# Performance work log

Hardware: AMD Instinct MI355X
Metric: run time of the kernel (lower is better)

The kernel has to match this reference:

```python
import jax, jax.numpy as jnp
import numpy as np

N = 65536      # batch rows
D = 32         # input_dim (number of per-feature sub-MLPs)
H = 128        # nodes_per_layer_in_sub_fn
# num_hidden_layers_per_feature_fn = 2 -> Linear(1,H),ReLU, Linear(H,H),ReLU, Linear(H,1)


def setup_inputs() -> dict:
    key = jax.random.key(0)
    ks = jax.random.split(key, 7)
    s1 = 1.0            # fan_in=1 kaiming-uniform-ish scale
    sH = 1.0 / np.sqrt(H)
    x = jax.random.normal(ks[0], (N, D), dtype=jnp.float32)
    W1 = jax.random.uniform(ks[1], (D, H), jnp.float32, -s1, s1)      # Linear(1,H) weight per feature
    b1 = jax.random.uniform(ks[2], (D, H), jnp.float32, -s1, s1)
    W2 = jax.random.uniform(ks[3], (D, H, H), jnp.float32, -sH, sH)   # Linear(H,H) per feature
    b2 = jax.random.uniform(ks[4], (D, H), jnp.float32, -sH, sH)
    W3 = jax.random.uniform(ks[5], (D, H), jnp.float32, -sH, sH)      # Linear(H,1) per feature
    b3 = jax.random.uniform(ks[6], (D,), jnp.float32, -sH, sH)
    return {"x": x, "W1": W1, "b1": b1, "W2": W2, "b2": b2, "W3": W3, "b3": b3}


def reference(x, W1, b1, W2, b2, W3, b3):
    # h1[n,d,h] = relu(x[n,d] * W1[d,h] + b1[d,h])
    h1 = jax.nn.relu(x[:, :, None] * W1[None, :, :] + b1[None, :, :])          # [N,D,H]
    # h2: per-feature batched GEMM, Linear(H,H) + ReLU
    h2 = jax.nn.relu(jnp.einsum('ndh,dhk->ndk', h1, W2) + b2[None, :, :])      # [N,D,H]
    # per-feature output Linear(H,1), then sum across features, keepdim
    per_feat = jnp.einsum('ndh,dh->nd', h2, W3) + b3[None, :]                  # [N,D]
    return jnp.sum(per_feat, axis=1, keepdims=True)                            # [N,1]
```

## Files before the change

### kernel.cpp

```cpp
#include <hip/hip_runtime.h>
#include <hip/hip_bf16.h>
#include <stdint.h>


#define D_FEAT 32
#define H_DIM  128
#define SLOTS  16
#define THREADS 256
#define RPB    4096
#define ITERS  32

typedef float    f32x16 __attribute__((ext_vector_type(16)));
typedef short    bf16x8 __attribute__((ext_vector_type(8)));
typedef uint32_t u32;

static __device__ __forceinline__ u32 cvtpk(float lo, float hi) {
    u32 r;
    asm("v_cvt_pk_bf16_f32 %0, %1, %2" : "=v"(r) : "v"(lo), "v"(hi));
    return r;
}
static __device__ __forceinline__ bf16x8 frag4(u32 a, u32 b, u32 c, u32 d) {
    int4 t = make_int4((int)a, (int)b, (int)c, (int)d);
    return __builtin_bit_cast(bf16x8, t);
}
static __device__ __forceinline__ bf16x8 frag1(u32 a) { return frag4(a, 0u, 0u, 0u); }

#define MFMA32(A, B, C) __builtin_amdgcn_mfma_f32_32x32x16_bf16((A), (B), (C), 0, 0, 0)

static __device__ __forceinline__ bf16x8 relu_pack(const f32x16& v, int s) {
    u32 c0 = cvtpk(fmaxf(v[8*s+0], 0.f), fmaxf(v[8*s+1], 0.f));
    u32 c1 = cvtpk(fmaxf(v[8*s+2], 0.f), fmaxf(v[8*s+3], 0.f));
    u32 c2 = cvtpk(fmaxf(v[8*s+4], 0.f), fmaxf(v[8*s+5], 0.f));
    u32 c3 = cvtpk(fmaxf(v[8*s+6], 0.f), fmaxf(v[8*s+7], 0.f));
    return frag4(c0, c1, c2, c3);
}

__global__ __launch_bounds__(256) void kan_init_out(const float* __restrict__ b3,
                                                    float* __restrict__ out, int n) {
    int i = blockIdx.x * blockDim.x + threadIdx.x;
    float s = 0.f;
#pragma unroll
    for (int k = 0; k < D_FEAT; ++k) s += b3[k];
    if (i < n) out[i] = s;
}

__global__ __launch_bounds__(THREADS, 2) void kan_main(
    const float* __restrict__ x,
    const float* __restrict__ W1,
    const float* __restrict__ b1,
    const float* __restrict__ W2,
    const float* __restrict__ b2,
    const float* __restrict__ W3,
    float* __restrict__ out)
{
    __shared__ float xall[RPB];
    __shared__ u32 w3lds[2][8][4];

    const int tid   = threadIdx.x;
    const int d     = blockIdx.x / SLOTS;
    const int bslot = blockIdx.x % SLOTS;
    const int w     = tid >> 6;
    const int l     = tid & 63;
    const int l31   = l & 31;
    const int g     = l >> 5;
    const size_t rowbase = (size_t)bslot * RPB;

#pragma unroll
    for (int i = 0; i < RPB / THREADS; ++i) {
        int idx = tid + THREADS * i;
        xall[idx] = x[(rowbase + idx) * D_FEAT + d];
    }
    if (tid < 16) {
        int gg = tid >> 3, ks2 = tid & 7;
        const float* W3d = W3 + d * H_DIM;
#pragma unroll
        for (int p = 0; p < 4; ++p) {
            int e0 = 2 * p, e1 = 2 * p + 1;
            int k0 = 16 * ks2 + 4 * gg + (e0 & 3) + 8 * (e0 >> 2);
            int k1 = 16 * ks2 + 4 * gg + (e1 & 3) + 8 * (e1 >> 2);
            w3lds[gg][ks2][p] = cvtpk(W3d[k0], W3d[k1]);
        }
    }

    u32 w1b1[4], b2w[4];
#pragma unroll
    for (int mt = 0; mt < 4; ++mt) {
        int m = 32 * mt + l31;
        u32 v  = cvtpk(W1[d * H_DIM + m], b1[d * H_DIM + m]);
        u32 bb = cvtpk(b2[d * H_DIM + m], 0.0f);
        w1b1[mt] = g ? 0u : v;
        b2w[mt]  = g ? 0u : bb;
    }
    const u32 onesw = g ? 0u : 0x00003F80u;

    bf16x8 w2f[4][8];
    {
        const float* W2d = W2 + (size_t)d * H_DIM * H_DIM;
#pragma unroll
        for (int mo = 0; mo < 4; ++mo) {
            int mm = 32 * mo + l31;
#pragma unroll
            for (int ks = 0; ks < 8; ++ks) {
                u32 dw[4];
#pragma unroll
                for (int p = 0; p < 4; ++p) {
                    int e0 = 2 * p, e1 = 2 * p + 1;
                    int k0 = 16 * ks + 4 * g + (e0 & 3) + 8 * (e0 >> 2);
                    int k1 = 16 * ks + 4 * g + (e1 & 3) + 8 * (e1 >> 2);
                    dw[p] = cvtpk(W2d[(size_t)k0 * H_DIM + mm],
                                  W2d[(size_t)k1 * H_DIM + mm]);
                }
                w2f[mo][ks] = frag4(dw[0], dw[1], dw[2], dw[3]);
            }
        }
    }
    __syncthreads();

    const f32x16 zc = {};

    for (int t = 0; t < ITERS; ++t) {
        const int loff = t * 128 + 32 * w;
        float xv = xall[loff + l31];
        u32 xpk = g ? 0u : cvtpk(xv, 1.0f);
        bf16x8 Bx = frag1(xpk);

        bf16x8 bfr[8];
#pragma unroll
        for (int mt = 0; mt < 4; ++mt) {
            f32x16 d1 = MFMA32(frag1(w1b1[mt]), Bx, zc);
            bfr[2 * mt + 0] = relu_pack(d1, 0);
            bfr[2 * mt + 1] = relu_pack(d1, 1);
        }

        f32x16 acc2 = zc;
        const bf16x8 onesB = frag1(onesw);
#pragma unroll
        for (int pa = 0; pa < 2; ++pa) {
            f32x16 a0 = MFMA32(frag1(b2w[2 * pa + 0]), onesB, zc);
            f32x16 a1 = MFMA32(frag1(b2w[2 * pa + 1]), onesB, zc);
#pragma unroll
            for (int ks = 0; ks < 8; ++ks) {
                a0 = MFMA32(w2f[2 * pa + 0][ks], bfr[ks], a0);
                a1 = MFMA32(w2f[2 * pa + 1][ks], bfr[ks], a1);
            }
            {
                const int mo0 = 2 * pa + 0, mo1 = 2 * pa + 1;
                bf16x8 w3a, w3b, w3c, w3d;
                w3a = *reinterpret_cast<const bf16x8*>(&w3lds[g][2 * mo0 + 0][0]);
                w3b = *reinterpret_cast<const bf16x8*>(&w3lds[g][2 * mo0 + 1][0]);
                w3c = *reinterpret_cast<const bf16x8*>(&w3lds[g][2 * mo1 + 0][0]);
                w3d = *reinterpret_cast<const bf16x8*>(&w3lds[g][2 * mo1 + 1][0]);
                acc2 = MFMA32(w3a, relu_pack(a0, 0), acc2);
                acc2 = MFMA32(w3b, relu_pack(a0, 1), acc2);
                acc2 = MFMA32(w3c, relu_pack(a1, 0), acc2);
                acc2 = MFMA32(w3d, relu_pack(a1, 1), acc2);
            }
        }
        if (!g) atomicAdd(&out[rowbase + loff + l31], acc2[0]);
    }
}

extern "C" void kernel_launch(void* const* d_in, const int* in_sizes, int n_in,
                              void* d_out, int out_size, void* d_ws, size_t ws_size,
                              hipStream_t stream) {
    const float* x  = (const float*)d_in[0];
    const float* W1 = (const float*)d_in[1];
    const float* b1 = (const float*)d_in[2];
    const float* W2 = (const float*)d_in[3];
    const float* b2 = (const float*)d_in[4];
    const float* W3 = (const float*)d_in[5];
    const float* b3 = (const float*)d_in[6];
    float* out = (float*)d_out;
    const int N = in_sizes[0] / D_FEAT;

    kan_init_out<<<(N + 255) / 256, 256, 0, stream>>>(b3, out, N);
    kan_main<<<D_FEAT * SLOTS, THREADS, 0, stream>>>(x, W1, b1, W2, b2, W3, out);
}
```

Baseline: 157.1 us.

## Split output channels across waves, interleave layer GEMMs, replace W3 MFMA with FMA reduction

Each wave now holds only half of W2's output tiles (2 of 4 mo blocks), and two waves share a 32-row tile. This halves register pressure and raises occupancy to 3 blocks and 24 slots per feature. The layer-1 MFMA is interleaved with the layer-2 MFMAs, and the final W3 projection uses scalar FMAs plus a cross-half shuffle instead of extra MFMAs. The b3 init kernel is replaced by a memset, with b3 folded into the atomics from one block group. In exchange, the atomicAdd count doubles, each wave recomputes layer 1, and the row-tile distribution across blocks is uneven.

```diff
diff --git a/kernel.cpp b/kernel.cpp
--- a/kernel.cpp
+++ b/kernel.cpp
@@ -5,10 +5,10 @@
 
 #define D_FEAT 32
 #define H_DIM  128
-#define SLOTS  16
+#define SLOTS  24
 #define THREADS 256
-#define RPB    4096
-#define ITERS  32
+#define ROWTILES 1024
+#define MAXT   43
 
 typedef float    f32x16 __attribute__((ext_vector_type(16)));
 typedef short    bf16x8 __attribute__((ext_vector_type(8)));
@@ -35,70 +35,59 @@
     return frag4(c0, c1, c2, c3);
 }
 
-__global__ __launch_bounds__(256) void kan_init_out(const float* __restrict__ b3,
-                                                    float* __restrict__ out, int n) {
-    int i = blockIdx.x * blockDim.x + threadIdx.x;
-    float s = 0.f;
-#pragma unroll
-    for (int k = 0; k < D_FEAT; ++k) s += b3[k];
-    if (i < n) out[i] = s;
-}
-
-__global__ __launch_bounds__(THREADS, 2) void kan_main(
+__global__ __launch_bounds__(THREADS, 3) void kan_main(
     const float* __restrict__ x,
     const float* __restrict__ W1,
     const float* __restrict__ b1,
     const float* __restrict__ W2,
     const float* __restrict__ b2,
     const float* __restrict__ W3,
+    const float* __restrict__ b3,
     float* __restrict__ out)
 {
-    __shared__ float xall[RPB];
-    __shared__ u32 w3lds[2][8][4];
+    __shared__ float xall[MAXT * 64];
+    __shared__ float W3s[H_DIM];
 
     const int tid   = threadIdx.x;
     const int d     = blockIdx.x / SLOTS;
     const int bslot = blockIdx.x % SLOTS;
     const int w     = tid >> 6;
+    const int wm    = w >> 1;
+    const int wn    = w & 1;
     const int l     = tid & 63;
     const int l31   = l & 31;
     const int g     = l >> 5;
-    const size_t rowbase = (size_t)bslot * RPB;
 
+    const int ntile = (ROWTILES - 1 - bslot) / SLOTS + 1;
+
+    for (int idx = tid; idx < ntile * 64; idx += THREADS) {
+        int tl = idx >> 6;
+        xall[idx] = x[(size_t)((bslot + SLOTS * tl) * 64 + (idx & 63)) * D_FEAT + d];
+    }
+    if (tid < H_DIM) W3s[tid] = W3[d * H_DIM + tid];
+
+    float b3s = 0.f;
 #pragma unroll
-    for (int i = 0; i < RPB / THREADS; ++i) {
-        int idx = tid + THREADS * i;
-        xall[idx] = x[(rowbase + idx) * D_FEAT + d];
-    }
-    if (tid < 16) {
-        int gg = tid >> 3, ks2 = tid & 7;
-        const float* W3d = W3 + d * H_DIM;
-#pragma unroll
-        for (int p = 0; p < 4; ++p) {
-            int e0 = 2 * p, e1 = 2 * p + 1;
-            int k0 = 16 * ks2 + 4 * gg + (e0 & 3) + 8 * (e0 >> 2);
-            int k1 = 16 * ks2 + 4 * gg + (e1 & 3) + 8 * (e1 >> 2);
-            w3lds[gg][ks2][p] = cvtpk(W3d[k0], W3d[k1]);
-        }
-    }
+    for (int k = 0; k < D_FEAT; ++k) b3s += b3[k];
 
-    u32 w1b1[4], b2w[4];
+    const int mo0 = 2 * wm, mo1 = 2 * wm + 1;
+    u32 w1b1[4], b2w[2];
 #pragma unroll
     for (int mt = 0; mt < 4; ++mt) {
         int m = 32 * mt + l31;
-        u32 v  = cvtpk(W1[d * H_DIM + m], b1[d * H_DIM + m]);
-        u32 bb = cvtpk(b2[d * H_DIM + m], 0.0f);
+        u32 v = cvtpk(W1[d * H_DIM + m], b1[d * H_DIM + m]);
         w1b1[mt] = g ? 0u : v;
-        b2w[mt]  = g ? 0u : bb;
     }
-    const u32 onesw = g ? 0u : 0x00003F80u;
+    b2w[0] = g ? 0u : cvtpk(b2[d * H_DIM + 32 * mo0 + l31], 0.f);
+    b2w[1] = g ? 0u : cvtpk(b2[d * H_DIM + 32 * mo1 + l31], 0.f);
+    const bf16x8 onesB = frag1(g ? 0u : 0x00003F80u);
 
-    bf16x8 w2f[4][8];
+    bf16x8 w2f[2][8];
     {
         const float* W2d = W2 + (size_t)d * H_DIM * H_DIM;
 #pragma unroll
-        for (int mo = 0; mo < 4; ++mo) {
-            int mm = 32 * mo + l31;
+        for (int j = 0; j < 2; ++j) {
+            int mm = 32 * (mo0 + j) + l31;
 #pragma unroll
             for (int ks = 0; ks < 8; ++ks) {
                 u32 dw[4];
@@ -110,53 +99,51 @@
                     dw[p] = cvtpk(W2d[(size_t)k0 * H_DIM + mm],
                                   W2d[(size_t)k1 * H_DIM + mm]);
                 }
-                w2f[mo][ks] = frag4(dw[0], dw[1], dw[2], dw[3]);
+                w2f[j][ks] = frag4(dw[0], dw[1], dw[2], dw[3]);
             }
         }
     }
     __syncthreads();
 
     const f32x16 zc = {};
+    const bool addb3 = (d == 0) && (wm == 0);
 
-    for (int t = 0; t < ITERS; ++t) {
-        const int loff = t * 128 + 32 * w;
-        float xv = xall[loff + l31];
-        u32 xpk = g ? 0u : cvtpk(xv, 1.0f);
-        bf16x8 Bx = frag1(xpk);
+    for (int it = 0; it < ntile; ++it) {
+        const int rbase = (bslot + SLOTS * it) * 64 + 32 * wn;
+        float xv = xall[it * 64 + 32 * wn + l31];
+        bf16x8 Bx = frag1(g ? 0u : cvtpk(xv, 1.0f));
 
-        bf16x8 bfr[8];
+        f32x16 a0 = MFMA32(frag1(b2w[0]), onesB, zc);
+        f32x16 a1 = MFMA32(frag1(b2w[1]), onesB, zc);
+
 #pragma unroll
         for (int mt = 0; mt < 4; ++mt) {
             f32x16 d1 = MFMA32(frag1(w1b1[mt]), Bx, zc);
-            bfr[2 * mt + 0] = relu_pack(d1, 0);
-            bfr[2 * mt + 1] = relu_pack(d1, 1);
+            bf16x8 bl = relu_pack(d1, 0);
+            bf16x8 bh = relu_pack(d1, 1);
+            a0 = MFMA32(w2f[0][2 * mt + 0], bl, a0);
+            a1 = MFMA32(w2f[1][2 * mt + 0], bl, a1);
+            a0 = MFMA32(w2f[0][2 * mt + 1], bh, a0);
+            a1 = MFMA32(w2f[1][2 * mt + 1], bh, a1);
         }
 
-        f32x16 acc2 = zc;
-        const bf16x8 onesB = frag1(onesw);
+        float rs = 0.f;
 #pragma unroll
-        for (int pa = 0; pa < 2; ++pa) {
-            f32x16 a0 = MFMA32(frag1(b2w[2 * pa + 0]), onesB, zc);
-            f32x16 a1 = MFMA32(frag1(b2w[2 * pa + 1]), onesB, zc);
-#pragma unroll
-            for (int ks = 0; ks < 8; ++ks) {
-                a0 = MFMA32(w2f[2 * pa + 0][ks], bfr[ks], a0);
-                a1 = MFMA32(w2f[2 * pa + 1][ks], bfr[ks], a1);
-            }
-            {
-                const int mo0 = 2 * pa + 0, mo1 = 2 * pa + 1;
-                bf16x8 w3a, w3b, w3c, w3d;
-                w3a = *reinterpret_cast<const bf16x8*>(&w3lds[g][2 * mo0 + 0][0]);
-                w3b = *reinterpret_cast<const bf16x8*>(&w3lds[g][2 * mo0 + 1][0]);
-                w3c = *reinterpret_cast<const bf16x8*>(&w3lds[g][2 * mo1 + 0][0]);
-                w3d = *reinterpret_cast<const bf16x8*>(&w3lds[g][2 * mo1 + 1][0]);
-                acc2 = MFMA32(w3a, relu_pack(a0, 0), acc2);
-                acc2 = MFMA32(w3b, relu_pack(a0, 1), acc2);
-                acc2 = MFMA32(w3c, relu_pack(a1, 0), acc2);
-                acc2 = MFMA32(w3d, relu_pack(a1, 1), acc2);
-            }
+        for (int q = 0; q < 4; ++q) {
+            const float4 w3a = *reinterpret_cast<const float4*>(&W3s[32 * mo0 + 4 * g + 8 * q]);
+            const float4 w3b = *reinterpret_cast<const float4*>(&W3s[32 * mo1 + 4 * g + 8 * q]);
+            rs += fmaxf(a0[4 * q + 0], 0.f) * w3a.x;
+            rs += fmaxf(a0[4 * q + 1], 0.f) * w3a.y;
+            rs += fmaxf(a0[4 * q + 2], 0.f) * w3a.z;
+            rs += fmaxf(a0[4 * q + 3], 0.f) * w3a.w;
+            rs += fmaxf(a1[4 * q + 0], 0.f) * w3b.x;
+            rs += fmaxf(a1[4 * q + 1], 0.f) * w3b.y;
+            rs += fmaxf(a1[4 * q + 2], 0.f) * w3b.z;
+            rs += fmaxf(a1[4 * q + 3], 0.f) * w3b.w;
         }
-        if (!g) atomicAdd(&out[rowbase + loff + l31], acc2[0]);
+        rs += __shfl_xor(rs, 32, 64);
+        if (addb3) rs += b3s;
+        if (!g) atomicAdd(&out[rbase + l31], rs);
     }
 }
 
@@ -173,6 +160,6 @@
     float* out = (float*)d_out;
     const int N = in_sizes[0] / D_FEAT;
 
-    kan_init_out<<<(N + 255) / 256, 256, 0, stream>>>(b3, out, N);
-    kan_main<<<D_FEAT * SLOTS, THREADS, 0, stream>>>(x, W1, b1, W2, b2, W3, out);
+    hipMemsetAsync(out, 0, (size_t)N * sizeof(float), stream);
+    kan_main<<<D_FEAT * SLOTS, THREADS, 0, stream>>>(x, W1, b1, W2, b2, W3, b3, out);
 }
```

New measurement: 158.0 us. Within noise of the previous version (+0.5%).
